# Optimization experiments

Hardware: AMD Instinct MI355X
Metric: run time of the kernel (lower is better)

Reference implementation:

```python
import jax, jax.numpy as jnp
import numpy as np

EPS = 1e-5

def _bn_relu(y, g, b, m, v):
    # y: [N,C,H,W]; BN inference form + ReLU
    inv = g / jnp.sqrt(v + EPS)
    return jax.nn.relu(y * inv[:, None, None] + (b - m * inv)[:, None, None])

def _pw(x, w):
    # 1x1 conv == per-pixel matmul over channels. x: [N,Ci,H,W], w: [Co,Ci]
    return jnp.einsum('nchw,oc->nohw', x, w)

def setup_inputs() -> dict:
    key = jax.random.key(0)
    ks = jax.random.split(key, 24)
    N, H, W = 8, 512, 512
    chans = [3, 128, 64, 32, 16]
    d = {'x': jax.random.normal(ks[0], (N, 3, H, W), dtype=jnp.float32)}
    for i in range(4):
        ci, co = chans[i], chans[i + 1]
        j = i + 1
        d[f'w{j}'] = jax.random.normal(ks[1 + 5 * i], (co, ci), dtype=jnp.float32) * (1.0 / np.sqrt(ci))
        d[f'g{j}'] = jnp.ones((co,), dtype=jnp.float32) + 0.1 * jax.random.normal(ks[2 + 5 * i], (co,), dtype=jnp.float32)
        d[f'b{j}'] = 0.1 * jax.random.normal(ks[3 + 5 * i], (co,), dtype=jnp.float32)
        d[f'm{j}'] = 0.1 * jax.random.normal(ks[4 + 5 * i], (co,), dtype=jnp.float32)
        d[f'v{j}'] = jax.random.uniform(ks[5 + 5 * i], (co,), dtype=jnp.float32, minval=0.5, maxval=1.5)
    d['wh'] = jax.random.normal(ks[21], (1, 16), dtype=jnp.float32) * 0.25
    d['bh'] = jnp.zeros((1,), dtype=jnp.float32)
    return d

def reference(x, w1, g1, b1, m1, v1, w2, g2, b2, m2, v2, w3, g3, b3, m3, v3,
              w4, g4, b4, m4, v4, wh, bh):
    h = _bn_relu(_pw(x, w1), g1, b1, m1, v1)   # [N,128,H,W]
    h = _bn_relu(_pw(h, w2), g2, b2, m2, v2)   # [N,64,H,W]
    h = _bn_relu(_pw(h, w3), g3, b3, m3, v3)   # [N,32,H,W]
    h = _bn_relu(_pw(h, w4), g4, b4, m4, v4)   # [N,16,H,W]
    return _pw(h, wh) + bh[:, None, None]      # [N,1,H,W]
```

## Files before the change

kernel.cpp:

```cpp
#include <hip/hip_runtime.h>

constexpr int HWSZ = 512 * 512;
constexpr int NPIX = 8 * HWSZ;
constexpr float EPS = 1e-5f;
constexpr int ITERS = 16;
constexpr int GRID  = 1024;

constexpr int S1 = 16, S2 = 144, S3 = 80, S4 = 48;
constexpr int OFF_W1 = 0;
constexpr int OFF_W2 = 2048;
constexpr int OFF_W3 = 11264;
constexpr int OFF_W4 = 13824;
constexpr int F16_TOTAL = 15360;
constexpr int OFF_WH_F32 = F16_TOTAL / 2;
constexpr int OFF_BH_F32 = OFF_WH_F32 + 16;

typedef _Float16 half8  __attribute__((ext_vector_type(8)));
typedef _Float16 half2t __attribute__((ext_vector_type(2)));
typedef float    f32x16 __attribute__((ext_vector_type(16)));
typedef unsigned int uint4t __attribute__((ext_vector_type(4)));

#define MFMA32(a, b, c) __builtin_amdgcn_mfma_f32_32x32x16_f16((a), (b), (c), 0, 0, 0)

__global__ void fold_weights(
    const float* __restrict__ w1, const float* __restrict__ g1, const float* __restrict__ b1,
    const float* __restrict__ m1, const float* __restrict__ v1,
    const float* __restrict__ w2, const float* __restrict__ g2, const float* __restrict__ b2,
    const float* __restrict__ m2, const float* __restrict__ v2,
    const float* __restrict__ w3, const float* __restrict__ g3, const float* __restrict__ b3,
    const float* __restrict__ m3, const float* __restrict__ v3,
    const float* __restrict__ w4, const float* __restrict__ g4, const float* __restrict__ b4,
    const float* __restrict__ m4, const float* __restrict__ v4,
    const float* __restrict__ wh, const float* __restrict__ bh,
    void* __restrict__ wsv)
{
    _Float16* wsh = (_Float16*)wsv;
    float*    wsf = (float*)wsv;
    int idx = blockIdx.x * 256 + threadIdx.x;

    if (idx < 2048) {
        int co = idx >> 4, k = idx & 15;
        float inv = g1[co] / sqrtf(v1[co] + EPS);
        float val = (k < 3) ? w1[co * 3 + k] * inv
                  : (k == 3) ? (b1[co] - m1[co] * inv) : 0.0f;
        wsh[OFF_W1 + idx] = (_Float16)val;
    } else if (idx < 11264) {
        int i = idx - 2048;
        int co = i / S2, k = i - co * S2;
        float inv = g2[co] / sqrtf(v2[co] + EPS);
        float val = (k < 128) ? w2[co * 128 + k] * inv
                  : (k == 128) ? (b2[co] - m2[co] * inv) : 0.0f;
        wsh[OFF_W2 + i] = (_Float16)val;
    } else if (idx < 13824) {
        int i = idx - 11264;
        int co = i / S3, k = i - co * S3;
        float inv = g3[co] / sqrtf(v3[co] + EPS);
        float val = (k < 64) ? w3[co * 64 + k] * inv
                  : (k == 64) ? (b3[co] - m3[co] * inv) : 0.0f;
        wsh[OFF_W3 + i] = (_Float16)val;
    } else if (idx < F16_TOTAL) {
        int i = idx - 13824;
        int co = i / S4, k = i - co * S4;
        float val = 0.0f;
        if (co < 16) {
            float inv = g4[co] / sqrtf(v4[co] + EPS);
            val = (k < 32) ? w4[co * 32 + k] * inv
                : (k == 32) ? (b4[co] - m4[co] * inv) : 0.0f;
        }
        wsh[OFF_W4 + i] = (_Float16)val;
    } else if (idx < F16_TOTAL + 16) {
        wsf[OFF_WH_F32 + (idx - F16_TOTAL)] = wh[idx - F16_TOTAL];
    } else if (idx == F16_TOTAL + 16) {
        wsf[OFF_BH_F32] = bh[0];
    }
}

__device__ inline void repack_tile(const f32x16 d, bool hi, half8* out2) {
    unsigned p[8];
    #pragma unroll
    for (int w = 0; w < 8; ++w) {
        half2t t;
        t.x = (_Float16)fmaxf(d[2 * w], 0.0f);
        t.y = (_Float16)fmaxf(d[2 * w + 1], 0.0f);
        p[w] = __builtin_bit_cast(unsigned, t);
    }
    #pragma unroll
    for (int ks = 0; ks < 2; ++ks) {
        const int b = 4 * ks;
        unsigned t0 = hi ? p[b + 0] : p[b + 2];
        unsigned t1 = hi ? p[b + 1] : p[b + 3];
        unsigned r0 = (unsigned)__shfl_xor((int)t0, 32, 64);
        unsigned r1 = (unsigned)__shfl_xor((int)t1, 32, 64);
        uint4t f;
        f.x = hi ? r0 : p[b + 0];
        f.y = hi ? r1 : p[b + 1];
        f.z = hi ? p[b + 2] : r0;
        f.w = hi ? p[b + 3] : r1;
        out2[ks] = __builtin_bit_cast(half8, f);
    }
}

__device__ inline f32x16 zero16() {
    f32x16 z;
    #pragma unroll
    for (int i = 0; i < 16; ++i) z[i] = 0.0f;
    return z;
}

__global__ __launch_bounds__(256, 2) void mlp_mfma(
    const float* __restrict__ x, const void* __restrict__ wsv, float* __restrict__ out)
{
    const _Float16* wsh = (const _Float16*)wsv;
    const float*    wsf = (const float*)wsv;

    const int tid  = threadIdx.x;
    const int l    = tid & 63;
    const int g    = l >> 5;
    const bool hi  = (g != 0);
    const int col  = l & 31;
    const int wave = tid >> 6;
    const long wgid = (long)blockIdx.x * 4 + wave;

    half8 A1[4], A2[2][9], A3[5], A4[3];
    #pragma unroll
    for (int mt = 0; mt < 4; ++mt)
        A1[mt] = *(const half8*)(wsh + OFF_W1 + (col + 32 * mt) * S1 + 8 * g);
    #pragma unroll
    for (int mt = 0; mt < 2; ++mt)
        #pragma unroll
        for (int ks = 0; ks < 9; ++ks)
            A2[mt][ks] = *(const half8*)(wsh + OFF_W2 + (col + 32 * mt) * S2 + 16 * ks + 8 * g);
    #pragma unroll
    for (int ks = 0; ks < 5; ++ks)
        A3[ks] = *(const half8*)(wsh + OFF_W3 + col * S3 + 16 * ks + 8 * g);
    #pragma unroll
    for (int ks = 0; ks < 3; ++ks)
        A4[ks] = *(const half8*)(wsh + OFF_W4 + col * S4 + 16 * ks + 8 * g);

    float whv[8];
    #pragma unroll
    for (int e = 0; e < 8; ++e)
        whv[e] = wsf[OFF_WH_F32 + ((e & 3) + 8 * (e >> 2) + 4 * g)];
    const float bhv = wsf[OFF_BH_F32];

    uint4t bbu; bbu.x = (g == 0) ? 0x00003C00u : 0u; bbu.y = 0u; bbu.z = 0u; bbu.w = 0u;
    const half8 Bbias = __builtin_bit_cast(half8, bbu);

    float xc0, xc1, xc2;
    {
        long q = wgid * ITERS * 32 + col;
        int n = (int)(q >> 18); int p = (int)(q & (HWSZ - 1));
        const float* xb = x + (size_t)n * 3 * HWSZ + p;
        xc0 = xb[0]; xc1 = xb[HWSZ]; xc2 = xb[2 * HWSZ];
    }

    for (int it = 0; it < ITERS; ++it) {
        const long q = (wgid * ITERS + it) * 32 + col;

        half2t t01; t01.x = (_Float16)xc0; t01.y = (_Float16)xc1;
        half2t t23; t23.x = (_Float16)xc2; t23.y = (_Float16)1.0f;
        unsigned bw0 = __builtin_bit_cast(unsigned, t01);
        unsigned bw1 = __builtin_bit_cast(unsigned, t23);
        uint4t b1u; b1u.x = (g == 0) ? bw0 : 0u; b1u.y = (g == 0) ? bw1 : 0u; b1u.z = 0u; b1u.w = 0u;
        const half8 B1 = __builtin_bit_cast(half8, b1u);

        if (it + 1 < ITERS) {
            long q2 = q + 32;
            int n2 = (int)(q2 >> 18); int p2 = (int)(q2 & (HWSZ - 1));
            const float* xb2 = x + (size_t)n2 * 3 * HWSZ + p2;
            xc0 = xb2[0]; xc1 = xb2[HWSZ]; xc2 = xb2[2 * HWSZ];
        }

        half8 B2[8];
        #pragma unroll
        for (int h = 0; h < 2; ++h) {
            f32x16 a0 = MFMA32(A1[2 * h + 0], B1, zero16());
            f32x16 a1 = MFMA32(A1[2 * h + 1], B1, zero16());
            repack_tile(a0, hi, &B2[4 * h + 0]);
            repack_tile(a1, hi, &B2[4 * h + 2]);
        }

        f32x16 c20 = zero16(), c21 = zero16();
        #pragma unroll
        for (int ks = 0; ks < 8; ++ks) {
            c20 = MFMA32(A2[0][ks], B2[ks], c20);
            c21 = MFMA32(A2[1][ks], B2[ks], c21);
        }
        c20 = MFMA32(A2[0][8], Bbias, c20);
        c21 = MFMA32(A2[1][8], Bbias, c21);

        half8 B3[4];
        repack_tile(c20, hi, &B3[0]);
        repack_tile(c21, hi, &B3[2]);
        f32x16 c3 = zero16();
        #pragma unroll
        for (int ks = 0; ks < 4; ++ks) c3 = MFMA32(A3[ks], B3[ks], c3);
        c3 = MFMA32(A3[4], Bbias, c3);

        half8 B4[2];
        repack_tile(c3, hi, &B4[0]);
        f32x16 c4 = zero16();
        c4 = MFMA32(A4[0], B4[0], c4);
        c4 = MFMA32(A4[1], B4[1], c4);
        c4 = MFMA32(A4[2], Bbias, c4);

        float s = 0.0f;
        #pragma unroll
        for (int e = 0; e < 8; ++e) s = fmaf(whv[e], fmaxf(c4[e], 0.0f), s);
        float partner = __shfl_xor(s, 32, 64);
        float val = s + partner + bhv;
        if (l < 32) out[q] = val;
    }
}

extern "C" void kernel_launch(void* const* d_in, const int* in_sizes, int n_in,
                              void* d_out, int out_size, void* d_ws, size_t ws_size,
                              hipStream_t stream) {
    const float* x  = (const float*)d_in[0];
    const float* w1 = (const float*)d_in[1];
    const float* g1 = (const float*)d_in[2];
    const float* b1 = (const float*)d_in[3];
    const float* m1 = (const float*)d_in[4];
    const float* v1 = (const float*)d_in[5];
    const float* w2 = (const float*)d_in[6];
    const float* g2 = (const float*)d_in[7];
    const float* b2 = (const float*)d_in[8];
    const float* m2 = (const float*)d_in[9];
    const float* v2 = (const float*)d_in[10];
    const float* w3 = (const float*)d_in[11];
    const float* g3 = (const float*)d_in[12];
    const float* b3 = (const float*)d_in[13];
    const float* m3 = (const float*)d_in[14];
    const float* v3 = (const float*)d_in[15];
    const float* w4 = (const float*)d_in[16];
    const float* g4 = (const float*)d_in[17];
    const float* b4 = (const float*)d_in[18];
    const float* m4 = (const float*)d_in[19];
    const float* v4 = (const float*)d_in[20];
    const float* wh = (const float*)d_in[21];
    const float* bh = (const float*)d_in[22];

    fold_weights<<<64, 256, 0, stream>>>(w1, g1, b1, m1, v1,
                                         w2, g2, b2, m2, v2,
                                         w3, g3, b3, m3, v3,
                                         w4, g4, b4, m4, v4,
                                         wh, bh, d_ws);

    mlp_mfma<<<GRID, 256, 0, stream>>>(x, d_ws, (float*)d_out);
}
```

Measured before the change: 179.2 us.

## Stage folded weights in padded LDS instead of registers to raise occupancy

Folded fp16 weights are no longer held in per-thread registers. Each block copies them into shared memory, with row strides padded by 4 halves to avoid bank conflicts, and each MFMA reads its A operand from LDS. This frees registers so launch bounds can rise to 3 blocks per SM, and the grid doubles while per-wave iterations halve. Indexing is simplified to pointer increments, and the fp16 conversion uses the packed round-toward-zero instruction, which slightly changes rounding. The cost is extra LDS traffic per MFMA and a per-block preload plus barrier.

```diff
diff --git a/kernel.cpp b/kernel.cpp
--- a/kernel.cpp
+++ b/kernel.cpp
@@ -3,19 +3,20 @@
 constexpr int HWSZ = 512 * 512;
 constexpr int NPIX = 8 * HWSZ;
 constexpr float EPS = 1e-5f;
-constexpr int ITERS = 16;
-constexpr int GRID  = 1024;
-
-constexpr int S1 = 16, S2 = 144, S3 = 80, S4 = 48;
+constexpr int ITERS = 8;
+constexpr int GRID  = 2048;
+
+constexpr int S1 = 20, S2 = 148, S3 = 84, S4 = 52;
 constexpr int OFF_W1 = 0;
-constexpr int OFF_W2 = 2048;
-constexpr int OFF_W3 = 11264;
-constexpr int OFF_W4 = 13824;
-constexpr int F16_TOTAL = 15360;
+constexpr int OFF_W2 = 2560;
+constexpr int OFF_W3 = 12032;
+constexpr int OFF_W4 = 14720;
+constexpr int F16_TOTAL = 16384;
 constexpr int OFF_WH_F32 = F16_TOTAL / 2;
 constexpr int OFF_BH_F32 = OFF_WH_F32 + 16;
 
 typedef _Float16 half8  __attribute__((ext_vector_type(8)));
+typedef _Float16 half4  __attribute__((ext_vector_type(4)));
 typedef _Float16 half2t __attribute__((ext_vector_type(2)));
 typedef float    f32x16 __attribute__((ext_vector_type(16)));
 typedef unsigned int uint4t __attribute__((ext_vector_type(4)));
@@ -38,28 +39,28 @@
     float*    wsf = (float*)wsv;
     int idx = blockIdx.x * 256 + threadIdx.x;
 
-    if (idx < 2048) {
-        int co = idx >> 4, k = idx & 15;
+    if (idx < OFF_W2) {
+        int co = idx / S1, k = idx - co * S1;
         float inv = g1[co] / sqrtf(v1[co] + EPS);
         float val = (k < 3) ? w1[co * 3 + k] * inv
                   : (k == 3) ? (b1[co] - m1[co] * inv) : 0.0f;
-        wsh[OFF_W1 + idx] = (_Float16)val;
-    } else if (idx < 11264) {
-        int i = idx - 2048;
+        wsh[idx] = (_Float16)val;
+    } else if (idx < OFF_W3) {
+        int i = idx - OFF_W2;
         int co = i / S2, k = i - co * S2;
         float inv = g2[co] / sqrtf(v2[co] + EPS);
         float val = (k < 128) ? w2[co * 128 + k] * inv
                   : (k == 128) ? (b2[co] - m2[co] * inv) : 0.0f;
-        wsh[OFF_W2 + i] = (_Float16)val;
-    } else if (idx < 13824) {
-        int i = idx - 11264;
+        wsh[idx] = (_Float16)val;
+    } else if (idx < OFF_W4) {
+        int i = idx - OFF_W3;
         int co = i / S3, k = i - co * S3;
         float inv = g3[co] / sqrtf(v3[co] + EPS);
         float val = (k < 64) ? w3[co * 64 + k] * inv
                   : (k == 64) ? (b3[co] - m3[co] * inv) : 0.0f;
-        wsh[OFF_W3 + i] = (_Float16)val;
+        wsh[idx] = (_Float16)val;
     } else if (idx < F16_TOTAL) {
-        int i = idx - 13824;
+        int i = idx - OFF_W4;
         int co = i / S4, k = i - co * S4;
         float val = 0.0f;
         if (co < 16) {
@@ -67,7 +68,7 @@
             val = (k < 32) ? w4[co * 32 + k] * inv
                 : (k == 32) ? (b4[co] - m4[co] * inv) : 0.0f;
         }
-        wsh[OFF_W4 + i] = (_Float16)val;
+        wsh[idx] = (_Float16)val;
     } else if (idx < F16_TOTAL + 16) {
         wsf[OFF_WH_F32 + (idx - F16_TOTAL)] = wh[idx - F16_TOTAL];
     } else if (idx == F16_TOTAL + 16) {
@@ -75,13 +76,18 @@
     }
 }
 
+__device__ inline half8 ldsw(const _Float16* W, int off) {
+    half4 lo = *(const half4*)(W + off);
+    half4 hi = *(const half4*)(W + off + 4);
+    return half8{lo[0], lo[1], lo[2], lo[3], hi[0], hi[1], hi[2], hi[3]};
+}
+
 __device__ inline void repack_tile(const f32x16 d, bool hi, half8* out2) {
     unsigned p[8];
     #pragma unroll
     for (int w = 0; w < 8; ++w) {
-        half2t t;
-        t.x = (_Float16)fmaxf(d[2 * w], 0.0f);
-        t.y = (_Float16)fmaxf(d[2 * w + 1], 0.0f);
+        auto t = __builtin_amdgcn_cvt_pkrtz(fmaxf(d[2 * w], 0.0f),
+                                            fmaxf(d[2 * w + 1], 0.0f));
         p[w] = __builtin_bit_cast(unsigned, t);
     }
     #pragma unroll
@@ -107,11 +113,13 @@
     return z;
 }
 
-__global__ __launch_bounds__(256, 2) void mlp_mfma(
+__global__ __launch_bounds__(256, 3) void mlp_mfma(
     const float* __restrict__ x, const void* __restrict__ wsv, float* __restrict__ out)
 {
     const _Float16* wsh = (const _Float16*)wsv;
     const float*    wsf = (const float*)wsv;
+
+    __shared__ _Float16 WL[F16_TOTAL];
 
     const int tid  = threadIdx.x;
     const int l    = tid & 63;
@@ -119,23 +127,14 @@
     const bool hi  = (g != 0);
     const int col  = l & 31;
     const int wave = tid >> 6;
-    const long wgid = (long)blockIdx.x * 4 + wave;
-
-    half8 A1[4], A2[2][9], A3[5], A4[3];
-    #pragma unroll
-    for (int mt = 0; mt < 4; ++mt)
-        A1[mt] = *(const half8*)(wsh + OFF_W1 + (col + 32 * mt) * S1 + 8 * g);
-    #pragma unroll
-    for (int mt = 0; mt < 2; ++mt)
-        #pragma unroll
-        for (int ks = 0; ks < 9; ++ks)
-            A2[mt][ks] = *(const half8*)(wsh + OFF_W2 + (col + 32 * mt) * S2 + 16 * ks + 8 * g);
-    #pragma unroll
-    for (int ks = 0; ks < 5; ++ks)
-        A3[ks] = *(const half8*)(wsh + OFF_W3 + col * S3 + 16 * ks + 8 * g);
-    #pragma unroll
-    for (int ks = 0; ks < 3; ++ks)
-        A4[ks] = *(const half8*)(wsh + OFF_W4 + col * S4 + 16 * ks + 8 * g);
+    const int wgid = blockIdx.x * 4 + wave;
+
+    {
+        const half8* gsrc = (const half8*)wsh;
+        half8* ldst = (half8*)WL;
+        #pragma unroll
+        for (int r = 0; r < 8; ++r) ldst[tid + 256 * r] = gsrc[tid + 256 * r];
+    }
 
     float whv[8];
     #pragma unroll
@@ -143,20 +142,25 @@
         whv[e] = wsf[OFF_WH_F32 + ((e & 3) + 8 * (e >> 2) + 4 * g)];
     const float bhv = wsf[OFF_BH_F32];
 
+    __syncthreads();
+
+    const int a1a = S1 * col + 8 * g;
+    const int a2a = OFF_W2 + S2 * col + 8 * g;
+    const int a3a = OFF_W3 + S3 * col + 8 * g;
+    const int a4a = OFF_W4 + S4 * col + 8 * g;
+
     uint4t bbu; bbu.x = (g == 0) ? 0x00003C00u : 0u; bbu.y = 0u; bbu.z = 0u; bbu.w = 0u;
     const half8 Bbias = __builtin_bit_cast(half8, bbu);
 
-    float xc0, xc1, xc2;
-    {
-        long q = wgid * ITERS * 32 + col;
-        int n = (int)(q >> 18); int p = (int)(q & (HWSZ - 1));
-        const float* xb = x + (size_t)n * 3 * HWSZ + p;
-        xc0 = xb[0]; xc1 = xb[HWSZ]; xc2 = xb[2 * HWSZ];
-    }
+    const int q0 = wgid * (ITERS * 32);
+    const int n  = q0 >> 18;
+    const int p0 = q0 & (HWSZ - 1);
+    const float* xp = x + (size_t)n * 3 * HWSZ + p0 + col;
+    float* op = out + q0 + col;
+
+    float xc0 = xp[0], xc1 = xp[HWSZ], xc2 = xp[2 * HWSZ];
 
     for (int it = 0; it < ITERS; ++it) {
-        const long q = (wgid * ITERS + it) * 32 + col;
-
         half2t t01; t01.x = (_Float16)xc0; t01.y = (_Float16)xc1;
         half2t t23; t23.x = (_Float16)xc2; t23.y = (_Float16)1.0f;
         unsigned bw0 = __builtin_bit_cast(unsigned, t01);
@@ -165,17 +169,15 @@
         const half8 B1 = __builtin_bit_cast(half8, b1u);
 
         if (it + 1 < ITERS) {
-            long q2 = q + 32;
-            int n2 = (int)(q2 >> 18); int p2 = (int)(q2 & (HWSZ - 1));
-            const float* xb2 = x + (size_t)n2 * 3 * HWSZ + p2;
-            xc0 = xb2[0]; xc1 = xb2[HWSZ]; xc2 = xb2[2 * HWSZ];
+            xp += 32;
+            xc0 = xp[0]; xc1 = xp[HWSZ]; xc2 = xp[2 * HWSZ];
         }
 
         half8 B2[8];
         #pragma unroll
         for (int h = 0; h < 2; ++h) {
-            f32x16 a0 = MFMA32(A1[2 * h + 0], B1, zero16());
-            f32x16 a1 = MFMA32(A1[2 * h + 1], B1, zero16());
+            f32x16 a0 = MFMA32(ldsw(WL, a1a + 640 * (2 * h + 0)), B1, zero16());
+            f32x16 a1 = MFMA32(ldsw(WL, a1a + 640 * (2 * h + 1)), B1, zero16());
             repack_tile(a0, hi, &B2[4 * h + 0]);
             repack_tile(a1, hi, &B2[4 * h + 2]);
         }
@@ -183,33 +185,34 @@
         f32x16 c20 = zero16(), c21 = zero16();
         #pragma unroll
         for (int ks = 0; ks < 8; ++ks) {
-            c20 = MFMA32(A2[0][ks], B2[ks], c20);
-            c21 = MFMA32(A2[1][ks], B2[ks], c21);
-        }
-        c20 = MFMA32(A2[0][8], Bbias, c20);
-        c21 = MFMA32(A2[1][8], Bbias, c21);
+            c20 = MFMA32(ldsw(WL, a2a + 16 * ks),        B2[ks], c20);
+            c21 = MFMA32(ldsw(WL, a2a + 4736 + 16 * ks), B2[ks], c21);
+        }
+        c20 = MFMA32(ldsw(WL, a2a + 128),        Bbias, c20);
+        c21 = MFMA32(ldsw(WL, a2a + 4736 + 128), Bbias, c21);
 
         half8 B3[4];
         repack_tile(c20, hi, &B3[0]);
         repack_tile(c21, hi, &B3[2]);
         f32x16 c3 = zero16();
         #pragma unroll
-        for (int ks = 0; ks < 4; ++ks) c3 = MFMA32(A3[ks], B3[ks], c3);
-        c3 = MFMA32(A3[4], Bbias, c3);
+        for (int ks = 0; ks < 4; ++ks) c3 = MFMA32(ldsw(WL, a3a + 16 * ks), B3[ks], c3);
+        c3 = MFMA32(ldsw(WL, a3a + 64), Bbias, c3);
 
         half8 B4[2];
         repack_tile(c3, hi, &B4[0]);
         f32x16 c4 = zero16();
-        c4 = MFMA32(A4[0], B4[0], c4);
-        c4 = MFMA32(A4[1], B4[1], c4);
-        c4 = MFMA32(A4[2], Bbias, c4);
+        c4 = MFMA32(ldsw(WL, a4a +  0), B4[0], c4);
+        c4 = MFMA32(ldsw(WL, a4a + 16), B4[1], c4);
+        c4 = MFMA32(ldsw(WL, a4a + 32), Bbias, c4);
 
         float s = 0.0f;
         #pragma unroll
         for (int e = 0; e < 8; ++e) s = fmaf(whv[e], fmaxf(c4[e], 0.0f), s);
         float partner = __shfl_xor(s, 32, 64);
         float val = s + partner + bhv;
-        if (l < 32) out[q] = val;
+        if (l < 32) op[0] = val;
+        op += 32;
     }
 }
 
@@ -240,7 +243,7 @@
     const float* wh = (const float*)d_in[21];
     const float* bh = (const float*)d_in[22];
 
-    fold_weights<<<64, 256, 0, stream>>>(w1, g1, b1, m1, v1,
+    fold_weights<<<65, 256, 0, stream>>>(w1, g1, b1, m1, v1,
                                          w2, g2, b2, m2, v2,
                                          w3, g3, b3, m3, v3,
                                          w4, g4, b4, m4, v4,
```

After: 214.7 us. +19.8%, slower.
